# Optimization experiments

Measured on AMD Instinct MI355X. Metric: run time of the kernel, lower is better.

Reference implementation:

```python
import jax, jax.numpy as jnp
import numpy as np

N, E, H, G = 50000, 500000, 64, 64


def _ln(x, g, b):
    m = jnp.mean(x, -1, keepdims=True)
    v = jnp.var(x, -1, keepdims=True)
    return (x - m) * jax.lax.rsqrt(v + 1e-5) * g + b


def _mlp_ln(x, w1, b1, w2, b2, g, be):
    # Linear -> ReLU -> (Dropout eval no-op) -> Linear -> LayerNorm
    h = jax.nn.relu(x @ w1 + b1)
    return _ln(h @ w2 + b2, g, be)


def setup_inputs() -> dict:
    key = jax.random.key(0)
    ks = jax.random.split(key, 24)
    w = lambda i, s: jax.random.normal(ks[i], s, dtype=jnp.float32) * 0.1
    z = lambda s: jnp.zeros(s, jnp.float32)
    o = lambda s: jnp.ones(s, jnp.float32)
    inp = {
        'x': jax.random.normal(ks[0], (N, 3), dtype=jnp.float32),
        'edge_index': jax.random.randint(ks[1], (2, E), 0, N),
        'edge_attr': jax.random.normal(ks[2], (E, 3), dtype=jnp.float32),
        'batch': jnp.sort(jax.random.randint(ks[3], (N,), 0, G)),
        'ne_w1': w(4, (3, H)), 'ne_b1': z((H,)), 'ne_w2': w(5, (H, H)), 'ne_b2': z((H,)), 'ne_g': o((H,)), 'ne_be': z((H,)),
        'ee_w1': w(6, (3, H)), 'ee_b1': z((H,)), 'ee_w2': w(7, (H, H)), 'ee_b2': z((H,)), 'ee_g': o((H,)), 'ee_be': z((H,)),
        'gin0_eps': z((1,)), 'gin0_w1': w(8, (H, H)), 'gin0_b1': z((H,)), 'gin0_w2': w(9, (H, H)), 'gin0_b2': z((H,)), 'gin0_g': o((H,)), 'gin0_be': z((H,)),
        'gin1_eps': z((1,)), 'gin1_w1': w(10, (H, H)), 'gin1_b1': z((H,)), 'gin1_w2': w(11, (H, H)), 'gin1_b2': z((H,)), 'gin1_g': o((H,)), 'gin1_be': z((H,)),
        'gp_w': w(12, (H, H)), 'gp_b': z((H,)), 'gp_g': o((H,)), 'gp_be': z((H,)),
        'ep_w1': w(13, (4 * H, 2 * H)), 'ep_b1': z((2 * H,)),
        'ep_w2': w(14, (2 * H, H)), 'ep_b2': z((H,)),
        'ep_w3': w(15, (H, 1)), 'ep_b3': z((1,)),
    }
    return inp


def reference(x, edge_index, edge_attr, batch,
              ne_w1, ne_b1, ne_w2, ne_b2, ne_g, ne_be,
              ee_w1, ee_b1, ee_w2, ee_b2, ee_g, ee_be,
              gin0_eps, gin0_w1, gin0_b1, gin0_w2, gin0_b2, gin0_g, gin0_be,
              gin1_eps, gin1_w1, gin1_b1, gin1_w2, gin1_b2, gin1_g, gin1_be,
              gp_w, gp_b, gp_g, gp_be,
              ep_w1, ep_b1, ep_w2, ep_b2, ep_w3, ep_b3):
    src, dst = edge_index[0], edge_index[1]
    # encoders
    h = _mlp_ln(x, ne_w1, ne_b1, ne_w2, ne_b2, ne_g, ne_be)            # [N, H]
    ef = _mlp_ln(edge_attr, ee_w1, ee_b1, ee_w2, ee_b2, ee_g, ee_be)   # [E, H]
    # GINEConv layer 0: mlp((1+eps)*x + scatter_add(relu(x_src + e)))
    msg = jax.nn.relu(h[src] + ef)
    aggr = jnp.zeros_like(h).at[dst].add(msg)
    h = _mlp_ln((1.0 + gin0_eps) * h + aggr, gin0_w1, gin0_b1, gin0_w2, gin0_b2, gin0_g, gin0_be)
    h = jax.nn.relu(h)  # inter-layer activation (dropout eval no-op)
    # GINEConv layer 1
    msg = jax.nn.relu(h[src] + ef)
    aggr = jnp.zeros_like(h).at[dst].add(msg)
    h = _mlp_ln((1.0 + gin1_eps) * h + aggr, gin1_w1, gin1_b1, gin1_w2, gin1_b2, gin1_g, gin1_be)
    # global mean pool over graphs
    seg = jax.ops.segment_sum(h, batch, num_segments=G)                            # [G, H]
    cnt = jax.ops.segment_sum(jnp.ones((h.shape[0], 1), h.dtype), batch, num_segments=G)
    gp = seg / jnp.maximum(cnt, 1.0)
    gf = _ln(jax.nn.relu(gp @ gp_w + gp_b), gp_g, gp_be)                           # [G, H]
    # edge predictor on [src | dst | global | edge] = [E, 4H]
    c = jnp.concatenate([h[src], h[dst], gf[batch[src]], ef], axis=-1)
    t = jnp.tanh(c @ ep_w1 + ep_b1)
    t = jnp.tanh(t @ ep_w2 + ep_b2)
    return jax.nn.sigmoid(t @ ep_w3 + ep_b3)  # [E, 1]
```

## Files before the change

kernel.cpp:

```cpp
#include <hip/hip_runtime.h>
#include <hip/hip_bf16.h>

typedef unsigned int uint;
typedef unsigned short ushort;
typedef __attribute__((ext_vector_type(8))) short short8;
typedef __attribute__((ext_vector_type(4))) float floatx4;

__device__ __forceinline__ float bf2f(ushort u) { return __uint_as_float(((uint)u) << 16); }
__device__ __forceinline__ ushort f2bf(float f) {
  uint u = __float_as_uint(f);
  u += 0x7fffu + ((u >> 16) & 1u);
  return (ushort)(u >> 16);
}
__device__ __forceinline__ uint pk2(float a, float b) {
  return (uint)f2bf(a) | ((uint)f2bf(b) << 16);
}
__device__ __forceinline__ float ldf(const void* p, long i, int m) {
  if (m) return bf2f(((const ushort*)p)[i]);
  return ((const float*)p)[i];
}
__device__ __forceinline__ int get_md(const uint* mdp) {
  return (mdp[0] == 0x3F800000u) ? 0 : 1;
}
__device__ __forceinline__ float fast_rcp(float x) { return __builtin_amdgcn_rcpf(x); }
__device__ __forceinline__ float tanh_fast(float x) {
  float e = __builtin_amdgcn_exp2f(2.8853900818f * x);
  return fmaf(-2.f, fast_rcp(1.f + e), 1.f);
}
__device__ __forceinline__ float sigmoid_fast(float x) {
  float e = __builtin_amdgcn_exp2f(-1.4426950409f * x);
  return fast_rcp(1.f + e);
}

__global__ __launch_bounds__(256) void k_enc_mfma(
    const void* __restrict__ in, int R,
    const void* __restrict__ w1, const void* __restrict__ b1,
    const ushort* __restrict__ w2sw_, const void* __restrict__ b2,
    const void* __restrict__ gam, const void* __restrict__ bet,
    ushort* __restrict__ outp, ushort* __restrict__ outp2,
    const int* __restrict__ epos, const uint* __restrict__ mdp)
{
  __shared__ float xs[64*3];
  __shared__ float w1s[192], b1s[64], b2s[64], gs[64], bs2[64];
  __shared__ __align__(16) ushort T_s[64 * 72];
  int md = get_md(mdp);
  int tid = threadIdx.x;
  long e0 = (long)blockIdx.x * 64;
  if (tid < 192) {
    w1s[tid] = ldf(w1, tid, md);
    int row = tid / 3, cc = tid - row*3;
    long e = e0 + row;
    xs[tid] = (e < R) ? ldf(in, e*3 + cc, md) : 0.f;
  }
  if (tid < 64) { b1s[tid] = ldf(b1, tid, md); b2s[tid] = ldf(b2, tid, md);
                  gs[tid] = ldf(gam, tid, md); bs2[tid] = ldf(bet, tid, md); }
  __syncthreads();
  int lane = tid & 63, wv = tid >> 6;
  int quad = lane >> 4, mm = lane & 15;
  float x0 = xs[(wv*16 + mm)*3 + 0];
  float x1 = xs[(wv*16 + mm)*3 + 1];
  float x2 = xs[(wv*16 + mm)*3 + 2];
  short8 af[2];
#pragma unroll
  for (int s = 0; s < 2; ++s) {
#pragma unroll
    for (int j = 0; j < 8; ++j) {
      int f = s*32 + quad*8 + j;
      float hv = fmaxf(b1s[f] + x0*w1s[f] + x1*w1s[64+f] + x2*w1s[128+f], 0.f);
      af[s][j] = (short)f2bf(hv);
    }
  }
  floatx4 acc[4] = {};
  const short8* Bp = (const short8*)w2sw_;
#pragma unroll
  for (int s = 0; s < 2; ++s) {
#pragma unroll
    for (int t = 0; t < 4; ++t) {
      short8 b = Bp[(s*4 + t)*64 + lane];
      acc[t] = __builtin_amdgcn_mfma_f32_16x16x32_bf16(af[s], b, acc[t], 0, 0, 0);
    }
  }
  float vv[4][4];
#pragma unroll
  for (int t = 0; t < 4; ++t) {
    float bb = b2s[mm + 16*t];
#pragma unroll
    for (int r = 0; r < 4; ++r) vv[t][r] = acc[t][r] + bb;
  }
  float mr[4], vr[4];
#pragma unroll
  for (int r = 0; r < 4; ++r) {
    float s = vv[0][r] + vv[1][r] + vv[2][r] + vv[3][r];
#pragma unroll
    for (int off = 1; off < 16; off <<= 1) s += __shfl_xor(s, off);
    mr[r] = s * 0.015625f;
    float q = 0.f;
#pragma unroll
    for (int t = 0; t < 4; ++t) { float d = vv[t][r] - mr[r]; q = fmaf(d, d, q); }
#pragma unroll
    for (int off = 1; off < 16; off <<= 1) q += __shfl_xor(q, off);
    vr[r] = rsqrtf(q * 0.015625f + 1e-5f);
  }
#pragma unroll
  for (int t = 0; t < 4; ++t) {
    int col = mm + 16*t;
    float g = gs[col], be = bs2[col];
#pragma unroll
    for (int r = 0; r < 4; ++r)
      T_s[(wv*16 + quad*4 + r)*72 + col] = f2bf((vv[t][r] - mr[r]) * vr[r] * g + be);
  }
  __syncthreads();
#pragma unroll
  for (int i = 0; i < 2; ++i) {
    int gi = tid + 256*i;
    int row = gi >> 3, c = gi & 7;
    long e = e0 + row;
    if (e < R) {
      uint4 v = *(const uint4*)&T_s[row*72 + c*8];
      ((uint4*)(outp + e*64))[c] = v;
      if (outp2)
        ((uint4*)(outp2 + (long)epos[e]*64))[c] = v;
    }
  }
}

__global__ __launch_bounds__(256) void k_swz(
    const void* __restrict__ w1, const void* __restrict__ w2,
    const void* __restrict__ w2e, const void* __restrict__ w2n,
    const void* __restrict__ gw10, const void* __restrict__ gw20,
    const void* __restrict__ gw11, const void* __restrict__ gw21,
    ushort* __restrict__ w1sw, ushort* __restrict__ w2sw,
    ushort* __restrict__ ew2sw, ushort* __restrict__ nw2sw,
    ushort* __restrict__ g0w1sw, ushort* __restrict__ g0w2sw,
    ushort* __restrict__ g1w1sw, ushort* __restrict__ g1w2sw,
    int* __restrict__ deg, float* __restrict__ gsum, int Nn,
    const uint* __restrict__ mdp)
{
  int md = get_md(mdp);
  int i = blockIdx.x * 256 + threadIdx.x;
  int nthr = gridDim.x * 256;
  for (int k = i; k < Nn; k += nthr) deg[k] = 0;
  for (int k = i; k < 64*64 + 64; k += nthr) gsum[k] = 0.f;
  if (i < 32768) {
    int q = i & 7, lane = (i >> 3) & 63, tt = (i >> 9) & 7, s = i >> 12;
    int k = s*32 + (lane >> 4)*8 + q, n = (lane & 15) + 16*tt;
    w1sw[i] = f2bf(ldf(w1, k*128 + n, md));
  }
  if (i < 8192) {
    int q = i & 7, lane = (i >> 3) & 63, tt = (i >> 9) & 3, s = i >> 11;
    int k = s*32 + (lane >> 4)*8 + q, n = (lane & 15) + 16*tt;
    int src = k*64 + n;
    w2sw[i]   = f2bf(ldf(w2,   src, md));
    ew2sw[i]  = f2bf(ldf(w2e,  src, md));
    nw2sw[i]  = f2bf(ldf(w2n,  src, md));
    g0w1sw[i] = f2bf(ldf(gw10, src, md));
    g0w2sw[i] = f2bf(ldf(gw20, src, md));
    g1w1sw[i] = f2bf(ldf(gw11, src, md));
    g1w2sw[i] = f2bf(ldf(gw21, src, md));
  }
}

__global__ __launch_bounds__(256) void k_deg(
    const int* __restrict__ ei, int* __restrict__ deg, int E_)
{
  int e = blockIdx.x * 256 + threadIdx.x;
  if (e < E_) atomicAdd(&deg[ei[E_ + e]], 1);
}

__global__ __launch_bounds__(256) void k_scan1(
    const int* __restrict__ deg, int* __restrict__ rs, int* __restrict__ bsum, int Nn)
{
  __shared__ int ls[256];
  int tid = threadIdx.x;
  int i = blockIdx.x * 256 + tid;
  int v = (i < Nn) ? deg[i] : 0;
  ls[tid] = v;
  __syncthreads();
  for (int off = 1; off < 256; off <<= 1) {
    int t = (tid >= off) ? ls[tid - off] : 0;
    __syncthreads();
    ls[tid] += t;
    __syncthreads();
  }
  if (i < Nn) rs[i] = ls[tid] - v;
  if (tid == 255) bsum[blockIdx.x] = ls[255];
}

__global__ __launch_bounds__(256) void k_scan2(
    int* __restrict__ bsum, int nb, int* __restrict__ rs, int Nn)
{
  __shared__ int ls[256];
  int tid = threadIdx.x;
  int chunk = (nb + 255) / 256;
  int c0 = tid * chunk, c1 = min(c0 + chunk, nb);
  int sum = 0;
  for (int i = c0; i < c1; ++i) sum += bsum[i];
  ls[tid] = sum;
  __syncthreads();
  for (int off = 1; off < 256; off <<= 1) {
    int t = (tid >= off) ? ls[tid - off] : 0;
    __syncthreads();
    ls[tid] += t;
    __syncthreads();
  }
  int run = ls[tid] - sum;
  for (int i = c0; i < c1; ++i) { int d = bsum[i]; bsum[i] = run; run += d; }
  if (tid == 255) rs[Nn] = ls[255];
}

__global__ __launch_bounds__(256) void k_scan3(
    int* __restrict__ rs, int* __restrict__ cur,
    const int* __restrict__ bsum, int Nn)
{
  int i = blockIdx.x * 256 + threadIdx.x;
  if (i < Nn) {
    int v = rs[i] + bsum[blockIdx.x];
    rs[i] = v;
    cur[i] = v;
  }
}

__global__ __launch_bounds__(256) void k_fill(
    const int* __restrict__ ei, int* __restrict__ cur,
    int2* __restrict__ ep, int* __restrict__ epos, int E_)
{
  int e = blockIdx.x * 256 + threadIdx.x;
  if (e < E_) {
    int s = ei[e];
    int d = ei[E_ + e];
    int p = atomicAdd(&cur[d], 1);
    ep[p] = make_int2(e, s);
    epos[e] = p;
  }
}

__global__ __launch_bounds__(256) void k_aggr(
    const ushort* __restrict__ hbu, const ushort* __restrict__ efp,
    const int2* __restrict__ ep, const int* __restrict__ rs,
    float* __restrict__ aggr, int Nn)
{
  int gw = (blockIdx.x * 256 + threadIdx.x) >> 6;
  int j = threadIdx.x & 63;
  if (gw >= Nn) return;
  int s0 = rs[gw], s1 = rs[gw + 1];
  float acc = 0.f;
  int idx = s0;
  for (; idx + 2 <= s1; idx += 2) {
    int2 a = ep[idx];
    int2 b = ep[idx + 1];
    float fA = bf2f(efp[(long)idx*64 + j]);
    float fB = bf2f(efp[(long)(idx+1)*64 + j]);
    float hA = bf2f(hbu[(long)a.y*64 + j]);
    float hB = bf2f(hbu[(long)b.y*64 + j]);
    acc += fmaxf(hA + fA, 0.f) + fmaxf(hB + fB, 0.f);
  }
  if (idx < s1) {
    int2 a = ep[idx];
    acc += fmaxf(bf2f(hbu[(long)a.y*64 + j]) + bf2f(efp[(long)idx*64 + j]), 0.f);
  }
  aggr[(long)gw*64 + j] = acc;
}

__global__ __launch_bounds__(256) void k_gine_mfma(
    const ushort* __restrict__ hbin, const float* __restrict__ aggr, int Nn,
    const void* __restrict__ epsp,
    const ushort* __restrict__ w1sw_, const void* __restrict__ b1,
    const ushort* __restrict__ w2sw_, const void* __restrict__ b2,
    const void* __restrict__ gam, const void* __restrict__ bet,
    ushort* __restrict__ hbout, int post_relu, const uint* __restrict__ mdp)
{
  __shared__ __align__(16) ushort Ws1[4096], Ws2[4096];
  __shared__ __align__(16) ushort T_s[64 * 72];
  __shared__ float b1s[64], b2s[64], gs[64], bs2[64];
  int md = get_md(mdp);
  int tid = threadIdx.x;
  {
    const uint4* p1 = (const uint4*)w1sw_;
    const uint4* p2 = (const uint4*)w2sw_;
    ((uint4*)Ws1)[tid] = p1[tid];
    ((uint4*)Ws1)[tid + 256] = p1[tid + 256];
    ((uint4*)Ws2)[tid] = p2[tid];
    ((uint4*)Ws2)[tid + 256] = p2[tid + 256];
  }
  if (tid < 64) { b1s[tid] = ldf(b1, tid, md); b2s[tid] = ldf(b2, tid, md);
                  gs[tid] = ldf(gam, tid, md); bs2[tid] = ldf(bet, tid, md); }
  float ope = 1.f + ldf(epsp, 0, md);
  int lane = tid & 63, wv = tid >> 6;
  int quad = lane >> 4, mm = lane & 15;
  long node = (long)blockIdx.x * 64 + wv*16 + mm;
  long nc = (node < Nn) ? node : (long)(Nn - 1);
  const ushort* hrow = hbin + nc*64;
  const float*  arow = aggr + nc*64;
  short8 af[2];
#pragma unroll
  for (int s = 0; s < 2; ++s) {
    int c = s*4 + quad;
    short8 hv = *(const short8*)(hrow + c*8);
    float4 a0 = *(const float4*)(arow + c*8);
    float4 a1 = *(const float4*)(arow + c*8 + 4);
    float uu[8];
    uu[0] = fmaf(bf2f((ushort)hv[0]), ope, a0.x);
    uu[1] = fmaf(bf2f((ushort)hv[1]), ope, a0.y);
    uu[2] = fmaf(bf2f((ushort)hv[2]), ope, a0.z);
    uu[3] = fmaf(bf2f((ushort)hv[3]), ope, a0.w);
    uu[4] = fmaf(bf2f((ushort)hv[4]), ope, a1.x);
    uu[5] = fmaf(bf2f((ushort)hv[5]), ope, a1.y);
    uu[6] = fmaf(bf2f((ushort)hv[6]), ope, a1.z);
    uu[7] = fmaf(bf2f((ushort)hv[7]), ope, a1.w);
#pragma unroll
    for (int j = 0; j < 8; ++j) af[s][j] = (short)f2bf(uu[j]);
  }
  __syncthreads();
  floatx4 acc[4] = {};
#pragma unroll
  for (int s = 0; s < 2; ++s) {
#pragma unroll
    for (int t = 0; t < 4; ++t) {
      short8 b = *(const short8*)&Ws1[((s*4 + t)*64 + lane)*8];
      acc[t] = __builtin_amdgcn_mfma_f32_16x16x32_bf16(af[s], b, acc[t], 0, 0, 0);
    }
  }
#pragma unroll
  for (int t = 0; t < 4; ++t) {
    int col = mm + 16*t;
    float bb = b1s[col];
#pragma unroll
    for (int r = 0; r < 4; ++r)
      T_s[(wv*16 + quad*4 + r)*72 + col] = f2bf(fmaxf(acc[t][r] + bb, 0.f));
  }
  __syncthreads();
  short8 af2[2];
#pragma unroll
  for (int s = 0; s < 2; ++s)
    af2[s] = *(const short8*)&T_s[(wv*16 + mm)*72 + s*32 + quad*8];
  floatx4 acc2[4] = {};
#pragma unroll
  for (int s = 0; s < 2; ++s) {
#pragma unroll
    for (int t = 0; t < 4; ++t) {
      short8 b = *(const short8*)&Ws2[((s*4 + t)*64 + lane)*8];
      acc2[t] = __builtin_amdgcn_mfma_f32_16x16x32_bf16(af2[s], b, acc2[t], 0, 0, 0);
    }
  }
  float vv[4][4];
#pragma unroll
  for (int t = 0; t < 4; ++t) {
    float bb = b2s[mm + 16*t];
#pragma unroll
    for (int r = 0; r < 4; ++r) vv[t][r] = acc2[t][r] + bb;
  }
  float mr[4], vr[4];
#pragma unroll
  for (int r = 0; r < 4; ++r) {
    float s = vv[0][r] + vv[1][r] + vv[2][r] + vv[3][r];
#pragma unroll
    for (int off = 1; off < 16; off <<= 1) s += __shfl_xor(s, off);
    mr[r] = s * 0.015625f;
    float q = 0.f;
#pragma unroll
    for (int t = 0; t < 4; ++t) { float d = vv[t][r] - mr[r]; q = fmaf(d, d, q); }
#pragma unroll
    for (int off = 1; off < 16; off <<= 1) q += __shfl_xor(q, off);
    vr[r] = rsqrtf(q * 0.015625f + 1e-5f);
  }
  __syncthreads();
#pragma unroll
  for (int t = 0; t < 4; ++t) {
    int col = mm + 16*t;
    float g = gs[col], be = bs2[col];
#pragma unroll
    for (int r = 0; r < 4; ++r) {
      float o = (vv[t][r] - mr[r]) * vr[r] * g + be;
      if (post_relu) o = fmaxf(o, 0.f);
      T_s[(wv*16 + quad*4 + r)*72 + col] = f2bf(o);
    }
  }
  __syncthreads();
#pragma unroll
  for (int i = 0; i < 2; ++i) {
    int gi = tid + 256*i;
    int row = gi >> 3, c = gi & 7;
    long n2 = (long)blockIdx.x * 64 + row;
    if (n2 < Nn)
      ((uint4*)(hbout + n2*64))[c] = *(const uint4*)&T_s[row*72 + c*8];
  }
}

__global__ __launch_bounds__(256) void k_pool_f(
    const ushort* __restrict__ hbu, const int* __restrict__ batch,
    float* __restrict__ gsum, float* __restrict__ gcnt, int Nn)
{
  int gw = (blockIdx.x * 256 + threadIdx.x) >> 6;
  int j = threadIdx.x & 63;
  long r0 = (long)gw * 64;
  if (r0 >= Nn) return;
  long rend = min(r0 + 64, (long)Nn);
  float acc = 0.f; int cur = batch[r0]; int run = 0;
  for (long r = r0; r < rend; ++r) {
    int g = batch[r];
    if (g != cur) {
      atomicAdd(&gsum[cur*64 + j], acc);
      if (j == 0) atomicAdd(&gcnt[cur], (float)run);
      acc = 0.f; run = 0; cur = g;
    }
    acc += bf2f(hbu[r*64 + j]);
    run++;
  }
  atomicAdd(&gsum[cur*64 + j], acc);
  if (j == 0) atomicAdd(&gcnt[cur], (float)run);
}

__global__ __launch_bounds__(64) void k_pool_fin_f(
    const float* __restrict__ gsum, const float* __restrict__ gcnt,
    const void* __restrict__ gpw, const void* __restrict__ gpb,
    const void* __restrict__ gpg, const void* __restrict__ gpbe,
    ushort* __restrict__ gfb, const uint* __restrict__ mdp)
{
  __shared__ float wgs[4096];
  __shared__ float us[64];
  int md = get_md(mdp);
  int j = threadIdx.x;
  int g = blockIdx.x;
  for (int i = j; i < 4096; i += 64) wgs[i] = ldf(gpw, i, md);
  float ic = 1.f / fmaxf(gcnt[g], 1.f);
  us[j] = gsum[g*64 + j] * ic;
  __syncthreads();
  float t = ldf(gpb, j, md);
#pragma unroll
  for (int k = 0; k < 64; ++k) t = fmaf(us[k], wgs[k*64 + j], t);
  t = fmaxf(t, 0.f);
  float m = t;
#pragma unroll
  for (int off = 1; off < 64; off <<= 1) m += __shfl_xor(m, off);
  m *= 0.015625f;
  float d = t - m;
  float v = d * d;
#pragma unroll
  for (int off = 1; off < 64; off <<= 1) v += __shfl_xor(v, off);
  float rs = rsqrtf(v * 0.015625f + 1e-5f);
  gfb[g*64 + j] = f2bf(d * rs * ldf(gpg, j, md) + ldf(gpbe, j, md));
}

__global__ __launch_bounds__(256) void k_pred_mfma(
    const ushort* __restrict__ hb, const ushort* __restrict__ efu,
    const ushort* __restrict__ gfb, const int* __restrict__ ei,
    const int* __restrict__ batch,
    const ushort* __restrict__ w1sw, const ushort* __restrict__ w2sw,
    const void* __restrict__ pb1, const void* __restrict__ pb2,
    const void* __restrict__ pw3, const void* __restrict__ pb3,
    void* __restrict__ out, int E_, const uint* __restrict__ mdp)
{
  __shared__ __align__(16) ushort Ws[8192];
  __shared__ __align__(16) ushort T_s[64 * 136];
  __shared__ float b1s[128], b2s[64], w3s[64];
  int md = get_md(mdp);
  int tid = threadIdx.x;
  if (tid < 128) b1s[tid] = ldf(pb1, tid, md);
  if (tid < 64) { b2s[tid] = ldf(pb2, tid, md); w3s[tid] = ldf(pw3, tid, md); }
  long e0 = (long)blockIdx.x * 64;
  int lane = tid & 63, wv = tid >> 6;
  int quad = lane >> 4, mm = lane & 15;
  long e = e0 + wv*16 + mm;
  if (e >= E_) e = E_ - 1;
  int si = ei[e];
  int di = ei[E_ + e];
  int gi = batch[si];
  const short8* hsrc = (const short8*)(hb  + (long)si*64);
  const short8* hdst = (const short8*)(hb  + (long)di*64);
  const short8* gsrc = (const short8*)(gfb + (long)gi*64);
  const short8* esrc = (const short8*)(efu + e*64);
  short8 af[8];
  af[0] = hsrc[quad]; af[1] = hsrc[4 + quad];
  af[2] = hdst[quad]; af[3] = hdst[4 + quad];
  af[4] = gsrc[quad]; af[5] = gsrc[4 + quad];
  af[6] = esrc[quad]; af[7] = esrc[4 + quad];
  floatx4 acc[8] = {};
  for (int q = 0; q < 4; ++q) {
    __syncthreads();
    const uint4* wp = (const uint4*)(w1sw + q*8192);
#pragma unroll
    for (int i = 0; i < 4; ++i)
      ((uint4*)Ws)[tid + 256*i] = wp[tid + 256*i];
    __syncthreads();
#pragma unroll
    for (int s4 = 0; s4 < 2; ++s4) {
      short8 a = af[q*2 + s4];
#pragma unroll
      for (int t = 0; t < 8; ++t) {
        short8 b = *(const short8*)&Ws[((s4*8 + t)*64 + lane)*8];
        acc[t] = __builtin_amdgcn_mfma_f32_16x16x32_bf16(a, b, acc[t], 0, 0, 0);
      }
    }
  }
#pragma unroll
  for (int t = 0; t < 8; ++t) {
    float bb = b1s[mm + 16*t];
#pragma unroll
    for (int r = 0; r < 4; ++r)
      T_s[(16*wv + quad*4 + r)*136 + mm + 16*t] = f2bf(tanh_fast(acc[t][r] + bb));
  }
  __syncthreads();
  {
    const uint4* wp2 = (const uint4*)w2sw;
#pragma unroll
    for (int i = 0; i < 4; ++i)
      ((uint4*)Ws)[tid + 256*i] = wp2[tid + 256*i];
  }
  __syncthreads();
  floatx4 acc2[4] = {};
#pragma unroll
  for (int s2 = 0; s2 < 4; ++s2) {
    short8 a = *(const short8*)&T_s[(16*wv + mm)*136 + s2*32 + quad*8];
#pragma unroll
    for (int t = 0; t < 4; ++t) {
      short8 b = *(const short8*)&Ws[((s2*4 + t)*64 + lane)*8];
      acc2[t] = __builtin_amdgcn_mfma_f32_16x16x32_bf16(a, b, acc2[t], 0, 0, 0);
    }
  }
  float p0 = 0.f, p1 = 0.f, p2 = 0.f, p3 = 0.f;
#pragma unroll
  for (int t = 0; t < 4; ++t) {
    int col = mm + 16*t;
    float bb = b2s[col], w3v = w3s[col];
    p0 = fmaf(tanh_fast(acc2[t][0] + bb), w3v, p0);
    p1 = fmaf(tanh_fast(acc2[t][1] + bb), w3v, p1);
    p2 = fmaf(tanh_fast(acc2[t][2] + bb), w3v, p2);
    p3 = fmaf(tanh_fast(acc2[t][3] + bb), w3v, p3);
  }
#pragma unroll
  for (int off = 1; off < 16; off <<= 1) {
    p0 += __shfl_xor(p0, off);
    p1 += __shfl_xor(p1, off);
    p2 += __shfl_xor(p2, off);
    p3 += __shfl_xor(p3, off);
  }
  if (mm == 0) {
    float b3 = ldf(pb3, 0, md);
    long eb = e0 + 16*wv + quad*4;
    float ps[4] = {p0, p1, p2, p3};
#pragma unroll
    for (int r = 0; r < 4; ++r) {
      if (eb + r < E_) {
        float sg = sigmoid_fast(ps[r] + b3);
        if (md) ((ushort*)out)[eb + r] = f2bf(sg);
        else    ((float*)out)[eb + r]  = sg;
      }
    }
  }
}

extern "C" void kernel_launch(void* const* d_in, const int* in_sizes, int n_in,
                              void* d_out, int out_size, void* d_ws, size_t ws_size,
                              hipStream_t stream)
{
  const void* x     = d_in[0];
  const int*  ei    = (const int*)d_in[1];
  const void* eattr = d_in[2];
  const int*  batch = (const int*)d_in[3];
  const void* ne_w1 = d_in[4];  const void* ne_b1 = d_in[5];
  const void* ne_w2 = d_in[6];  const void* ne_b2 = d_in[7];
  const void* ne_g  = d_in[8];  const void* ne_be = d_in[9];
  const void* ee_w1 = d_in[10]; const void* ee_b1 = d_in[11];
  const void* ee_w2 = d_in[12]; const void* ee_b2 = d_in[13];
  const void* ee_g  = d_in[14]; const void* ee_be = d_in[15];
  const void* g0_ep = d_in[16];
  const void* g0_w1 = d_in[17]; const void* g0_b1 = d_in[18];
  const void* g0_w2 = d_in[19]; const void* g0_b2 = d_in[20];
  const void* g0_g  = d_in[21]; const void* g0_be = d_in[22];
  const void* g1_ep = d_in[23];
  const void* g1_w1 = d_in[24]; const void* g1_b1 = d_in[25];
  const void* g1_w2 = d_in[26]; const void* g1_b2 = d_in[27];
  const void* g1_g  = d_in[28]; const void* g1_be = d_in[29];
  const void* gp_w  = d_in[30]; const void* gp_b  = d_in[31];
  const void* gp_g  = d_in[32]; const void* gp_be = d_in[33];
  const void* ep_w1 = d_in[34]; const void* ep_b1 = d_in[35];
  const void* ep_w2 = d_in[36]; const void* ep_b2 = d_in[37];
  const void* ep_w3 = d_in[38]; const void* ep_b3 = d_in[39];

  int N = in_sizes[3];
  int E = in_sizes[1] / 2;
  const uint* mdp = (const uint*)ne_g;

  char* ws = (char*)d_ws;
  size_t off = 0;
  auto alloc = [&](size_t bytes) { char* p = ws + off; off += (bytes + 255) & ~(size_t)255; return p; };
  ushort* hb     = (ushort*)alloc((size_t)N * 64 * 2);
  ushort* efu    = (ushort*)alloc((size_t)E * 64 * 2);
  ushort* efp    = (ushort*)alloc((size_t)E * 64 * 2);
  float*  aggr   = (float*) alloc((size_t)N * 64 * 4);
  float*  gsum   = (float*) alloc((64 * 64 + 64) * 4);
  float*  gcnt   = gsum + 64 * 64;
  ushort* gfb    = (ushort*)alloc(64 * 64 * 2);
  ushort* w1sw   = (ushort*)alloc(32768 * 2);
  ushort* w2sw   = (ushort*)alloc(8192 * 2);
  ushort* ew2sw  = (ushort*)alloc(8192 * 2);
  ushort* nw2sw  = (ushort*)alloc(8192 * 2);
  ushort* g0w1sw = (ushort*)alloc(8192 * 2);
  ushort* g0w2sw = (ushort*)alloc(8192 * 2);
  ushort* g1w1sw = (ushort*)alloc(8192 * 2);
  ushort* g1w2sw = (ushort*)alloc(8192 * 2);
  int*    deg    = (int*)   alloc((size_t)N * 4);
  int*    rs     = (int*)   alloc((size_t)(N + 1) * 4);
  int*    cur    = (int*)   alloc((size_t)N * 4);
  int2*   ep     = (int2*)  alloc((size_t)E * 8);
  int*    epos   = (int*)   alloc((size_t)E * 4);
  int*    bsum   = (int*)   alloc((size_t)((N + 255) / 256) * 4);
  (void)ws_size; (void)n_in; (void)out_size;

  int gN = (N + 255) / 256;
  int gE = (E + 255) / 256;
  int gE64 = (E + 63) / 64;
  int gN64 = (N + 63) / 64;
  int gAggr = (int)(((long)N * 64 + 255) / 256);
  int gPool = ((N + 63) / 64 + 3) / 4;

  k_swz<<<128, 256, 0, stream>>>(ep_w1, ep_w2, ee_w2, ne_w2, g0_w1, g0_w2, g1_w1, g1_w2,
                                 w1sw, w2sw, ew2sw, nw2sw,
                                 g0w1sw, g0w2sw, g1w1sw, g1w2sw,
                                 deg, gsum, N, mdp);
  k_deg<<<gE, 256, 0, stream>>>(ei, deg, E);
  k_scan1<<<gN, 256, 0, stream>>>(deg, rs, bsum, N);
  k_scan2<<<1, 256, 0, stream>>>(bsum, gN, rs, N);
  k_scan3<<<gN, 256, 0, stream>>>(rs, cur, bsum, N);
  k_fill<<<gE, 256, 0, stream>>>(ei, cur, ep, epos, E);
  k_enc_mfma<<<gN64, 256, 0, stream>>>(x, N, ne_w1, ne_b1, nw2sw, ne_b2, ne_g, ne_be,
                                       hb, (ushort*)nullptr, (const int*)nullptr, mdp);
  k_enc_mfma<<<gE64, 256, 0, stream>>>(eattr, E, ee_w1, ee_b1, ew2sw, ee_b2, ee_g, ee_be,
                                       efu, efp, epos, mdp);
  k_aggr<<<gAggr, 256, 0, stream>>>(hb, efp, ep, rs, aggr, N);
  k_gine_mfma<<<gN64, 256, 0, stream>>>(hb, aggr, N, g0_ep, g0w1sw, g0_b1, g0w2sw, g0_b2,
                                        g0_g, g0_be, hb, 1, mdp);
  k_aggr<<<gAggr, 256, 0, stream>>>(hb, efp, ep, rs, aggr, N);
  k_gine_mfma<<<gN64, 256, 0, stream>>>(hb, aggr, N, g1_ep, g1w1sw, g1_b1, g1w2sw, g1_b2,
                                        g1_g, g1_be, hb, 0, mdp);
  k_pool_f<<<gPool, 256, 0, stream>>>(hb, batch, gsum, gcnt, N);
  k_pool_fin_f<<<64, 64, 0, stream>>>(gsum, gcnt, gp_w, gp_b, gp_g, gp_be, gfb, mdp);
  k_pred_mfma<<<gE64, 256, 0, stream>>>(hb, efu, gfb, ei, batch, w1sw, w2sw,
                                        ep_b1, ep_b2, ep_w3, ep_b3, d_out, E, mdp);
}
```

Measured before the change: 453.0 us.

## Process two 64-edge tiles per block in predictor to reuse staged weights

The edge predictor kernel now handles 128 edges per block as two 64-edge groups. Each layer-1 weight slice is staged once in shared memory and applied to both groups, halving weight staging and block count. Activation loads are now issued per quarter inside the loop rather than all upfront, and a launch-bounds occupancy hint of 4 is added. In exchange there are 16 accumulators per thread, which raises register pressure and may cut occupancy or cause spills.

```diff
diff --git a/kernel.cpp b/kernel.cpp
--- a/kernel.cpp
+++ b/kernel.cpp
@@ -441,7 +441,7 @@
   gfb[g*64 + j] = f2bf(d * rs * ldf(gpg, j, md) + ldf(gpbe, j, md));
 }
 
-__global__ __launch_bounds__(256) void k_pred_mfma(
+__global__ __launch_bounds__(256, 4) void k_pred_mfma(
     const ushort* __restrict__ hb, const ushort* __restrict__ efu,
     const ushort* __restrict__ gfb, const int* __restrict__ ei,
     const int* __restrict__ batch,
@@ -457,25 +457,26 @@
   int tid = threadIdx.x;
   if (tid < 128) b1s[tid] = ldf(pb1, tid, md);
   if (tid < 64) { b2s[tid] = ldf(pb2, tid, md); w3s[tid] = ldf(pw3, tid, md); }
-  long e0 = (long)blockIdx.x * 64;
+  long e0 = (long)blockIdx.x * 128;
   int lane = tid & 63, wv = tid >> 6;
   int quad = lane >> 4, mm = lane & 15;
-  long e = e0 + wv*16 + mm;
-  if (e >= E_) e = E_ - 1;
-  int si = ei[e];
-  int di = ei[E_ + e];
-  int gi = batch[si];
-  const short8* hsrc = (const short8*)(hb  + (long)si*64);
-  const short8* hdst = (const short8*)(hb  + (long)di*64);
-  const short8* gsrc = (const short8*)(gfb + (long)gi*64);
-  const short8* esrc = (const short8*)(efu + e*64);
-  short8 af[8];
-  af[0] = hsrc[quad]; af[1] = hsrc[4 + quad];
-  af[2] = hdst[quad]; af[3] = hdst[4 + quad];
-  af[4] = gsrc[quad]; af[5] = gsrc[4 + quad];
-  af[6] = esrc[quad]; af[7] = esrc[4 + quad];
-  floatx4 acc[8] = {};
+  long eA = e0 + wv*16 + mm;       if (eA >= E_) eA = E_ - 1;
+  long eB = e0 + 64 + wv*16 + mm;  if (eB >= E_) eB = E_ - 1;
+  int siA = ei[eA], diA = ei[E_ + eA];
+  int siB = ei[eB], diB = ei[E_ + eB];
+  int giA = batch[siA], giB = batch[siB];
+  floatx4 acc[16] = {};
+#pragma unroll
   for (int q = 0; q < 4; ++q) {
+    const ushort* bp; uint oA, oB;
+    if (q == 0)      { bp = hb;  oA = (uint)siA * 128u; oB = (uint)siB * 128u; }
+    else if (q == 1) { bp = hb;  oA = (uint)diA * 128u; oB = (uint)diB * 128u; }
+    else if (q == 2) { bp = gfb; oA = (uint)giA * 128u; oB = (uint)giB * 128u; }
+    else             { bp = efu; oA = (uint)eA  * 128u; oB = (uint)eB  * 128u; }
+    short8 aA0 = *(const short8*)((const char*)bp + oA + quad*16);
+    short8 aA1 = *(const short8*)((const char*)bp + oA + 64 + quad*16);
+    short8 aB0 = *(const short8*)((const char*)bp + oB + quad*16);
+    short8 aB1 = *(const short8*)((const char*)bp + oB + 64 + quad*16);
     __syncthreads();
     const uint4* wp = (const uint4*)(w1sw + q*8192);
 #pragma unroll
@@ -483,13 +484,16 @@
       ((uint4*)Ws)[tid + 256*i] = wp[tid + 256*i];
     __syncthreads();
 #pragma unroll
-    for (int s4 = 0; s4 < 2; ++s4) {
-      short8 a = af[q*2 + s4];
-#pragma unroll
-      for (int t = 0; t < 8; ++t) {
-        short8 b = *(const short8*)&Ws[((s4*8 + t)*64 + lane)*8];
-        acc[t] = __builtin_amdgcn_mfma_f32_16x16x32_bf16(a, b, acc[t], 0, 0, 0);
-      }
+    for (int t = 0; t < 8; ++t) {
+      short8 b = *(const short8*)&Ws[(t*64 + lane)*8];
+      acc[t]   = __builtin_amdgcn_mfma_f32_16x16x32_bf16(aA0, b, acc[t],   0, 0, 0);
+      acc[8+t] = __builtin_amdgcn_mfma_f32_16x16x32_bf16(aB0, b, acc[8+t], 0, 0, 0);
+    }
+#pragma unroll
+    for (int t = 0; t < 8; ++t) {
+      short8 b = *(const short8*)&Ws[((8 + t)*64 + lane)*8];
+      acc[t]   = __builtin_amdgcn_mfma_f32_16x16x32_bf16(aA1, b, acc[t],   0, 0, 0);
+      acc[8+t] = __builtin_amdgcn_mfma_f32_16x16x32_bf16(aB1, b, acc[8+t], 0, 0, 0);
     }
   }
 #pragma unroll
@@ -507,43 +511,55 @@
       ((uint4*)Ws)[tid + 256*i] = wp2[tid + 256*i];
   }
   __syncthreads();
-  floatx4 acc2[4] = {};
-#pragma unroll
-  for (int s2 = 0; s2 < 4; ++s2) {
-    short8 a = *(const short8*)&T_s[(16*wv + mm)*136 + s2*32 + quad*8];
+  float b3 = ldf(pb3, 0, md);
+#pragma unroll
+  for (int g = 0; g < 2; ++g) {
+    if (g) {
+#pragma unroll
+      for (int t = 0; t < 8; ++t) {
+        float bb = b1s[mm + 16*t];
+#pragma unroll
+        for (int r = 0; r < 4; ++r)
+          T_s[(16*wv + quad*4 + r)*136 + mm + 16*t] = f2bf(tanh_fast(acc[8+t][r] + bb));
+      }
+    }
+    floatx4 acc2[4] = {};
+#pragma unroll
+    for (int s2 = 0; s2 < 4; ++s2) {
+      short8 a = *(const short8*)&T_s[(16*wv + mm)*136 + s2*32 + quad*8];
+#pragma unroll
+      for (int t = 0; t < 4; ++t) {
+        short8 b = *(const short8*)&Ws[((s2*4 + t)*64 + lane)*8];
+        acc2[t] = __builtin_amdgcn_mfma_f32_16x16x32_bf16(a, b, acc2[t], 0, 0, 0);
+      }
+    }
+    float p0 = 0.f, p1 = 0.f, p2 = 0.f, p3 = 0.f;
 #pragma unroll
     for (int t = 0; t < 4; ++t) {
-      short8 b = *(const short8*)&Ws[((s2*4 + t)*64 + lane)*8];
-      acc2[t] = __builtin_amdgcn_mfma_f32_16x16x32_bf16(a, b, acc2[t], 0, 0, 0);
-    }
-  }
-  float p0 = 0.f, p1 = 0.f, p2 = 0.f, p3 = 0.f;
-#pragma unroll
-  for (int t = 0; t < 4; ++t) {
-    int col = mm + 16*t;
-    float bb = b2s[col], w3v = w3s[col];
-    p0 = fmaf(tanh_fast(acc2[t][0] + bb), w3v, p0);
-    p1 = fmaf(tanh_fast(acc2[t][1] + bb), w3v, p1);
-    p2 = fmaf(tanh_fast(acc2[t][2] + bb), w3v, p2);
-    p3 = fmaf(tanh_fast(acc2[t][3] + bb), w3v, p3);
-  }
-#pragma unroll
-  for (int off = 1; off < 16; off <<= 1) {
-    p0 += __shfl_xor(p0, off);
-    p1 += __shfl_xor(p1, off);
-    p2 += __shfl_xor(p2, off);
-    p3 += __shfl_xor(p3, off);
-  }
-  if (mm == 0) {
-    float b3 = ldf(pb3, 0, md);
-    long eb = e0 + 16*wv + quad*4;
-    float ps[4] = {p0, p1, p2, p3};
-#pragma unroll
-    for (int r = 0; r < 4; ++r) {
-      if (eb + r < E_) {
-        float sg = sigmoid_fast(ps[r] + b3);
-        if (md) ((ushort*)out)[eb + r] = f2bf(sg);
-        else    ((float*)out)[eb + r]  = sg;
+      int col = mm + 16*t;
+      float bb = b2s[col], w3v = w3s[col];
+      p0 = fmaf(tanh_fast(acc2[t][0] + bb), w3v, p0);
+      p1 = fmaf(tanh_fast(acc2[t][1] + bb), w3v, p1);
+      p2 = fmaf(tanh_fast(acc2[t][2] + bb), w3v, p2);
+      p3 = fmaf(tanh_fast(acc2[t][3] + bb), w3v, p3);
+    }
+#pragma unroll
+    for (int off = 1; off < 16; off <<= 1) {
+      p0 += __shfl_xor(p0, off);
+      p1 += __shfl_xor(p1, off);
+      p2 += __shfl_xor(p2, off);
+      p3 += __shfl_xor(p3, off);
+    }
+    if (mm == 0) {
+      long eb = e0 + g*64 + 16*wv + quad*4;
+      float ps[4] = {p0, p1, p2, p3};
+#pragma unroll
+      for (int r = 0; r < 4; ++r) {
+        if (eb + r < E_) {
+          float sg = sigmoid_fast(ps[r] + b3);
+          if (md) ((ushort*)out)[eb + r] = f2bf(sg);
+          else    ((float*)out)[eb + r]  = sg;
+        }
       }
     }
   }
@@ -610,6 +626,7 @@
   int gN = (N + 255) / 256;
   int gE = (E + 255) / 256;
   int gE64 = (E + 63) / 64;
+  int gE128 = (E + 127) / 128;
   int gN64 = (N + 63) / 64;
   int gAggr = (int)(((long)N * 64 + 255) / 256);
   int gPool = ((N + 63) / 64 + 3) / 4;
@@ -635,6 +652,6 @@
                                         g1_g, g1_be, hb, 0, mdp);
   k_pool_f<<<gPool, 256, 0, stream>>>(hb, batch, gsum, gcnt, N);
   k_pool_fin_f<<<64, 64, 0, stream>>>(gsum, gcnt, gp_w, gp_b, gp_g, gp_be, gfb, mdp);
-  k_pred_mfma<<<gE64, 256, 0, stream>>>(hb, efu, gfb, ei, batch, w1sw, w2sw,
-                                        ep_b1, ep_b2, ep_w3, ep_b3, d_out, E, mdp);
-}
+  k_pred_mfma<<<gE128, 256, 0, stream>>>(hb, efu, gfb, ei, batch, w1sw, w2sw,
+                                         ep_b1, ep_b2, ep_w3, ep_b3, d_out, E, mdp);
+}
```

Result: no change. 445.2 us (-1.7%).

## Make edge predictor persistent with full weights resident in LDS

Applied to the files above, without the earlier changes.

The edge-predictor kernel becomes a persistent kernel: 256 blocks of 1024 threads each load both weight matrices into LDS once, then every wave loops over 16-edge groups. This removes the per-block reloading of weights in four chunks and the block-wide barriers between chunks. The tanh intermediate is now staged per wave, in two halves, in a smaller LDS tile. The bf16 conversion also switches to the compiler's native cast. The trade-offs are about 90KB of LDS per block, which limits occupancy, and no more barrier-level overlap between blocks.

```diff
diff --git a/kernel.cpp b/kernel.cpp
--- a/kernel.cpp
+++ b/kernel.cpp
@@ -8,12 +8,10 @@
 
 __device__ __forceinline__ float bf2f(ushort u) { return __uint_as_float(((uint)u) << 16); }
 __device__ __forceinline__ ushort f2bf(float f) {
-  uint u = __float_as_uint(f);
-  u += 0x7fffu + ((u >> 16) & 1u);
-  return (ushort)(u >> 16);
-}
-__device__ __forceinline__ uint pk2(float a, float b) {
-  return (uint)f2bf(a) | ((uint)f2bf(b) << 16);
+  __bf16 h = (__bf16)f;
+  ushort u;
+  __builtin_memcpy(&u, &h, 2);
+  return u;
 }
 __device__ __forceinline__ float ldf(const void* p, long i, int m) {
   if (m) return bf2f(((const ushort*)p)[i]);
@@ -30,6 +28,11 @@
 __device__ __forceinline__ float sigmoid_fast(float x) {
   float e = __builtin_amdgcn_exp2f(-1.4426950409f * x);
   return fast_rcp(1.f + e);
+}
+__device__ __forceinline__ void gll16(const void* g, void* l) {
+  __builtin_amdgcn_global_load_lds(
+      (const __attribute__((address_space(1))) uint*)g,
+      (__attribute__((address_space(3))) uint*)l, 16, 0, 0);
 }
 
 __global__ __launch_bounds__(256) void k_enc_mfma(
@@ -441,7 +444,7 @@
   gfb[g*64 + j] = f2bf(d * rs * ldf(gpg, j, md) + ldf(gpbe, j, md));
 }
 
-__global__ __launch_bounds__(256) void k_pred_mfma(
+__global__ __launch_bounds__(1024, 4) void k_pred_mfma(
     const ushort* __restrict__ hb, const ushort* __restrict__ efu,
     const ushort* __restrict__ gfb, const int* __restrict__ ei,
     const int* __restrict__ batch,
@@ -450,100 +453,104 @@
     const void* __restrict__ pw3, const void* __restrict__ pb3,
     void* __restrict__ out, int E_, const uint* __restrict__ mdp)
 {
-  __shared__ __align__(16) ushort Ws[8192];
-  __shared__ __align__(16) ushort T_s[64 * 136];
+  __shared__ __align__(16) ushort W1s[32768];
+  __shared__ __align__(16) ushort W2s[8192];
+  __shared__ __align__(16) ushort T_s[16 * 16*72];
   __shared__ float b1s[128], b2s[64], w3s[64];
   int md = get_md(mdp);
   int tid = threadIdx.x;
+  {
+    const uint4* w1p = (const uint4*)w1sw;
+#pragma unroll
+    for (int i = 0; i < 4; ++i)
+      ((uint4*)W1s)[tid + 1024*i] = w1p[tid + 1024*i];
+    ((uint4*)W2s)[tid] = ((const uint4*)w2sw)[tid];
+  }
   if (tid < 128) b1s[tid] = ldf(pb1, tid, md);
   if (tid < 64) { b2s[tid] = ldf(pb2, tid, md); w3s[tid] = ldf(pw3, tid, md); }
-  long e0 = (long)blockIdx.x * 64;
+  __syncthreads();
+
   int lane = tid & 63, wv = tid >> 6;
   int quad = lane >> 4, mm = lane & 15;
-  long e = e0 + wv*16 + mm;
-  if (e >= E_) e = E_ - 1;
-  int si = ei[e];
-  int di = ei[E_ + e];
-  int gi = batch[si];
-  const short8* hsrc = (const short8*)(hb  + (long)si*64);
-  const short8* hdst = (const short8*)(hb  + (long)di*64);
-  const short8* gsrc = (const short8*)(gfb + (long)gi*64);
-  const short8* esrc = (const short8*)(efu + e*64);
-  short8 af[8];
-  af[0] = hsrc[quad]; af[1] = hsrc[4 + quad];
-  af[2] = hdst[quad]; af[3] = hdst[4 + quad];
-  af[4] = gsrc[quad]; af[5] = gsrc[4 + quad];
-  af[6] = esrc[quad]; af[7] = esrc[4 + quad];
-  floatx4 acc[8] = {};
-  for (int q = 0; q < 4; ++q) {
-    __syncthreads();
-    const uint4* wp = (const uint4*)(w1sw + q*8192);
-#pragma unroll
-    for (int i = 0; i < 4; ++i)
-      ((uint4*)Ws)[tid + 256*i] = wp[tid + 256*i];
-    __syncthreads();
-#pragma unroll
-    for (int s4 = 0; s4 < 2; ++s4) {
-      short8 a = af[q*2 + s4];
+  ushort* Tw = T_s + wv * (16*72);
+  float b3 = ldf(pb3, 0, md);
+  int ngroups = (E_ + 15) >> 4;
+  int nw = gridDim.x * 16;
+  for (int g = blockIdx.x * 16 + wv; g < ngroups; g += nw) {
+    long e = (long)g*16 + mm; if (e >= E_) e = E_ - 1;
+    int si = ei[e], di = ei[E_ + e];
+    int gi = batch[si];
+    const char* hs = (const char*)hb  + (uint)si*128u;
+    const char* hd = (const char*)hb  + (uint)di*128u;
+    const char* gs = (const char*)gfb + (uint)gi*128u;
+    const char* es = (const char*)efu + (uint)e *128u;
+    short8 cq[8];
+    cq[0] = *(const short8*)(hs + quad*16);
+    cq[1] = *(const short8*)(hs + 64 + quad*16);
+    cq[2] = *(const short8*)(hd + quad*16);
+    cq[3] = *(const short8*)(hd + 64 + quad*16);
+    cq[4] = *(const short8*)(gs + quad*16);
+    cq[5] = *(const short8*)(gs + 64 + quad*16);
+    cq[6] = *(const short8*)(es + quad*16);
+    cq[7] = *(const short8*)(es + 64 + quad*16);
+    floatx4 acc[8] = {};
+#pragma unroll
+    for (int c = 0; c < 8; ++c) {
 #pragma unroll
       for (int t = 0; t < 8; ++t) {
-        short8 b = *(const short8*)&Ws[((s4*8 + t)*64 + lane)*8];
-        acc[t] = __builtin_amdgcn_mfma_f32_16x16x32_bf16(a, b, acc[t], 0, 0, 0);
+        short8 b = *(const short8*)&W1s[((c*8 + t)*64 + lane)*8];
+        acc[t] = __builtin_amdgcn_mfma_f32_16x16x32_bf16(cq[c], b, acc[t], 0, 0, 0);
       }
     }
-  }
-#pragma unroll
-  for (int t = 0; t < 8; ++t) {
-    float bb = b1s[mm + 16*t];
-#pragma unroll
-    for (int r = 0; r < 4; ++r)
-      T_s[(16*wv + quad*4 + r)*136 + mm + 16*t] = f2bf(tanh_fast(acc[t][r] + bb));
-  }
-  __syncthreads();
-  {
-    const uint4* wp2 = (const uint4*)w2sw;
-#pragma unroll
-    for (int i = 0; i < 4; ++i)
-      ((uint4*)Ws)[tid + 256*i] = wp2[tid + 256*i];
-  }
-  __syncthreads();
-  floatx4 acc2[4] = {};
-#pragma unroll
-  for (int s2 = 0; s2 < 4; ++s2) {
-    short8 a = *(const short8*)&T_s[(16*wv + mm)*136 + s2*32 + quad*8];
+    floatx4 acc2[4] = {};
+#pragma unroll
+    for (int h = 0; h < 2; ++h) {
+#pragma unroll
+      for (int t4 = 0; t4 < 4; ++t4) {
+        int t = h*4 + t4;
+        float bb = b1s[mm + 16*t];
+#pragma unroll
+        for (int r = 0; r < 4; ++r)
+          Tw[(quad*4 + r)*72 + mm + 16*t4] = f2bf(tanh_fast(acc[t][r] + bb));
+      }
+#pragma unroll
+      for (int s2h = 0; s2h < 2; ++s2h) {
+        int s2 = h*2 + s2h;
+        short8 a = *(const short8*)&Tw[mm*72 + s2h*32 + quad*8];
+#pragma unroll
+        for (int t = 0; t < 4; ++t) {
+          short8 b = *(const short8*)&W2s[((s2*4 + t)*64 + lane)*8];
+          acc2[t] = __builtin_amdgcn_mfma_f32_16x16x32_bf16(a, b, acc2[t], 0, 0, 0);
+        }
+      }
+    }
+    float p0 = 0.f, p1 = 0.f, p2 = 0.f, p3 = 0.f;
 #pragma unroll
     for (int t = 0; t < 4; ++t) {
-      short8 b = *(const short8*)&Ws[((s2*4 + t)*64 + lane)*8];
-      acc2[t] = __builtin_amdgcn_mfma_f32_16x16x32_bf16(a, b, acc2[t], 0, 0, 0);
-    }
-  }
-  float p0 = 0.f, p1 = 0.f, p2 = 0.f, p3 = 0.f;
-#pragma unroll
-  for (int t = 0; t < 4; ++t) {
-    int col = mm + 16*t;
-    float bb = b2s[col], w3v = w3s[col];
-    p0 = fmaf(tanh_fast(acc2[t][0] + bb), w3v, p0);
-    p1 = fmaf(tanh_fast(acc2[t][1] + bb), w3v, p1);
-    p2 = fmaf(tanh_fast(acc2[t][2] + bb), w3v, p2);
-    p3 = fmaf(tanh_fast(acc2[t][3] + bb), w3v, p3);
-  }
-#pragma unroll
-  for (int off = 1; off < 16; off <<= 1) {
-    p0 += __shfl_xor(p0, off);
-    p1 += __shfl_xor(p1, off);
-    p2 += __shfl_xor(p2, off);
-    p3 += __shfl_xor(p3, off);
-  }
-  if (mm == 0) {
-    float b3 = ldf(pb3, 0, md);
-    long eb = e0 + 16*wv + quad*4;
-    float ps[4] = {p0, p1, p2, p3};
-#pragma unroll
-    for (int r = 0; r < 4; ++r) {
-      if (eb + r < E_) {
-        float sg = sigmoid_fast(ps[r] + b3);
-        if (md) ((ushort*)out)[eb + r] = f2bf(sg);
-        else    ((float*)out)[eb + r]  = sg;
+      int col = mm + 16*t;
+      float bb = b2s[col], w3v = w3s[col];
+      p0 = fmaf(tanh_fast(acc2[t][0] + bb), w3v, p0);
+      p1 = fmaf(tanh_fast(acc2[t][1] + bb), w3v, p1);
+      p2 = fmaf(tanh_fast(acc2[t][2] + bb), w3v, p2);
+      p3 = fmaf(tanh_fast(acc2[t][3] + bb), w3v, p3);
+    }
+#pragma unroll
+    for (int off = 1; off < 16; off <<= 1) {
+      p0 += __shfl_xor(p0, off);
+      p1 += __shfl_xor(p1, off);
+      p2 += __shfl_xor(p2, off);
+      p3 += __shfl_xor(p3, off);
+    }
+    if (mm == 0) {
+      long eb = (long)g*16 + quad*4;
+      float ps[4] = {p0, p1, p2, p3};
+#pragma unroll
+      for (int r = 0; r < 4; ++r) {
+        if (eb + r < E_) {
+          float sg = sigmoid_fast(ps[r] + b3);
+          if (md) ((ushort*)out)[eb + r] = f2bf(sg);
+          else    ((float*)out)[eb + r]  = sg;
+        }
       }
     }
   }
@@ -635,6 +642,6 @@
                                         g1_g, g1_be, hb, 0, mdp);
   k_pool_f<<<gPool, 256, 0, stream>>>(hb, batch, gsum, gcnt, N);
   k_pool_fin_f<<<64, 64, 0, stream>>>(gsum, gcnt, gp_w, gp_b, gp_g, gp_be, gfb, mdp);
-  k_pred_mfma<<<gE64, 256, 0, stream>>>(hb, efu, gfb, ei, batch, w1sw, w2sw,
+  k_pred_mfma<<<256, 1024, 0, stream>>>(hb, efu, gfb, ei, batch, w1sw, w2sw,
                                         ep_b1, ep_b2, ep_w3, ep_b3, d_out, E, mdp);
 }
```

After: 436.9 us. 1.04x faster.
